# Kernel tuning notes

Hardware: AMD Instinct MI355X
Metric: run time of the kernel (lower is better)

Reference implementation:

```python
import jax, jax.numpy as jnp
import numpy as np

NUM_HEADS = 16


def trinity_mask(txt_tok, img_tok):
    """Boolean [N, N] mask, True = attend. Faithful to get_mask(..., 'trinity'):
    - image rows attend block-diagonally within 3 equal image chunks
    - text rows attend to all image tokens and causally to text tokens.
    """
    assert img_tok % 3 == 0, "Invalid text token sizes"
    sit = img_tok // 3
    N = txt_tok + img_tok
    i = jnp.arange(N)[:, None]
    j = jnp.arange(N)[None, :]
    img_img = (i < img_tok) & (j < img_tok) & ((i // sit) == (j // sit))
    txt_img = (i >= img_tok) & (j < img_tok)
    txt_txt = (i >= img_tok) & (j >= img_tok) & (i >= j)
    return img_img | txt_img | txt_txt


def setup_inputs() -> dict:
    key = jax.random.key(0)
    ks = jax.random.split(key, 12)
    B, TXT, IMG = 4, 512, 1536
    N = TXT + IMG
    DQ, DKV = 1024, 1024
    s = lambda d: 1.0 / np.sqrt(d).astype(np.float32)
    return {
        "q": jax.random.normal(ks[0], (B, N, DQ), jnp.float32),
        "kv": jax.random.normal(ks[1], (B, N, DKV), jnp.float32),
        "Wq": jax.random.normal(ks[2], (DQ, DQ), jnp.float32) * s(DQ),
        "bq": jnp.zeros((DQ,), jnp.float32),
        "Wk": jax.random.normal(ks[3], (DKV, DQ), jnp.float32) * s(DKV),
        "bk": jnp.zeros((DQ,), jnp.float32),
        "Wv": jax.random.normal(ks[4], (DKV, DQ), jnp.float32) * s(DKV),
        "bv": jnp.zeros((DQ,), jnp.float32),
        "Wo": jax.random.normal(ks[5], (DQ, DQ), jnp.float32) * s(DQ),
        "bo": jnp.zeros((DQ,), jnp.float32),
        "txt_tok_len": TXT,
        "img_tok_len": IMG,
    }


def reference(q, kv, Wq, bq, Wk, bk, Wv, bv, Wo, bo, txt_tok_len, img_tok_len):
    B, N, C = q.shape
    H = NUM_HEADS
    d = C // H
    scale = d ** -0.5
    # projections, split heads: [B, H, N, d]
    qh = (q @ Wq + bq).reshape(B, N, H, d).transpose(0, 2, 1, 3)
    kh = (kv @ Wk + bk).reshape(B, N, H, d).transpose(0, 2, 1, 3)
    vh = (kv @ Wv + bv).reshape(B, N, H, d).transpose(0, 2, 1, 3)
    scores = jnp.einsum("bhqd,bhkd->bhqk", qh, kh) * scale
    mask = trinity_mask(txt_tok_len, img_tok_len)  # [N, N] bool
    scores = jnp.where(mask[None, None], scores, -jnp.inf)
    attn = jax.nn.softmax(scores, axis=-1)
    # dropout in eval mode -> identity
    out = jnp.einsum("bhqk,bhkd->bhqd", attn, vh)
    out = out.transpose(0, 2, 1, 3).reshape(B, N, C)
    return out @ Wo + bo
```

## Files before the change

kernel.cpp:

```cpp
#include <hip/hip_runtime.h>


typedef _Float16 h16;
typedef _Float16 f16x8 __attribute__((ext_vector_type(8)));
typedef float f32x4 __attribute__((ext_vector_type(4)));

#define BATCH 4
#define NTOK  2048
#define CDIM  1024
#define NHEAD 16
#define HDIM  64
#define IMGTOK 1536
#define MROWS (BATCH * NTOK)

__device__ __forceinline__ void gload_lds16(const void* g, void* l) {
  __builtin_amdgcn_global_load_lds(
      (const __attribute__((address_space(1))) unsigned int*)g,
      (__attribute__((address_space(3))) unsigned int*)l, 16, 0, 0);
}

__global__ __launch_bounds__(256)
void cvt_f16(const float* __restrict__ s, h16* __restrict__ d) {
  size_t i = ((size_t)blockIdx.x * 256 + threadIdx.x) * 8;
  float4 a = *(const float4*)(s + i);
  float4 b = *(const float4*)(s + i + 4);
  f16x8 o;
  o[0] = (h16)a.x; o[1] = (h16)a.y; o[2] = (h16)a.z; o[3] = (h16)a.w;
  o[4] = (h16)b.x; o[5] = (h16)b.y; o[6] = (h16)b.z; o[7] = (h16)b.w;
  *(f16x8*)(d + i) = o;
}

__global__ __launch_bounds__(256)
void wtrans(const float* __restrict__ W0, const float* __restrict__ W1,
            const float* __restrict__ W2, const float* __restrict__ W3,
            h16* __restrict__ T0, h16* __restrict__ T1,
            h16* __restrict__ T2, h16* __restrict__ T3) {
  const float* W; h16* T;
  switch (blockIdx.z) {
    case 0: W = W0; T = T0; break;
    case 1: W = W1; T = T1; break;
    case 2: W = W2; T = T2; break;
    default: W = W3; T = T3; break;
  }
  __shared__ float t[32][33];
  const int n0 = blockIdx.x * 32, k0 = blockIdx.y * 32;
  const int tx = threadIdx.x, ty = threadIdx.y;
#pragma unroll
  for (int i = 0; i < 4; i++)
    t[ty + 8 * i][tx] = W[(size_t)(k0 + ty + 8 * i) * CDIM + n0 + tx];
  __syncthreads();
#pragma unroll
  for (int i = 0; i < 4; i++)
    T[(size_t)(n0 + ty + 8 * i) * CDIM + k0 + tx] = (h16)t[tx][ty + 8 * i];
}

template <int MODE>
__global__ __launch_bounds__(256)
void gemm_bt(const h16* __restrict__ X, const h16* __restrict__ WT,
             const float* __restrict__ bias, void* __restrict__ outp) {
  __shared__ __attribute__((aligned(16))) h16 smem[4 * 8192];
  const int tid = threadIdx.x;
  const int lane = tid & 63;
  const int w = tid >> 6;
  const int wr = w >> 1, wc = w & 1;
  const int l15 = lane & 15, lhi = lane >> 4;
  const int m0 = blockIdx.y * 128;
  const int n0 = blockIdx.x * 128;

  f32x4 acc[4][4] = {};

  const int sr = tid >> 2;
  const int pc = tid & 3;
  const int lc = pc ^ ((sr >> 1) & 3);
  const h16* gA0 = X + (size_t)(m0 + sr) * CDIM + lc * 8;
  const h16* gA1 = gA0 + (size_t)64 * CDIM;
  const h16* gB0 = WT + (size_t)(n0 + sr) * CDIM + lc * 8;
  const h16* gB1 = gB0 + (size_t)64 * CDIM;

#define GSTAGE(bi, kt)                                      \
  do {                                                      \
    h16* A_ = smem + (bi) * 8192;                           \
    h16* B_ = A_ + 4096;                                    \
    gload_lds16(gA0 + (kt) * 32, A_ + tid * 8);             \
    gload_lds16(gA1 + (kt) * 32, A_ + (256 + tid) * 8);     \
    gload_lds16(gB0 + (kt) * 32, B_ + tid * 8);             \
    gload_lds16(gB1 + (kt) * 32, B_ + (256 + tid) * 8);     \
  } while (0)

  const int NT = CDIM / 32;
  GSTAGE(0, 0);
  GSTAGE(1, 1);
  GSTAGE(2, 2);
  const int rswz = (l15 >> 1) & 3;

  for (int kt = 0; kt < NT; ++kt) {
    if (kt + 2 < NT)      asm volatile("s_waitcnt vmcnt(8)" ::: "memory");
    else if (kt + 1 < NT) asm volatile("s_waitcnt vmcnt(4)" ::: "memory");
    else                  asm volatile("s_waitcnt vmcnt(0)" ::: "memory");
    __builtin_amdgcn_s_barrier();
    if (kt + 3 < NT) GSTAGE((kt + 3) & 3, kt + 3);
    const h16* A_ = smem + (kt & 3) * 8192;
    const h16* B_ = A_ + 4096;
    f16x8 a[4], bb[4];
#pragma unroll
    for (int i = 0; i < 4; i++)
      a[i] = *(const f16x8*)(A_ + (wr * 64 + i * 16 + l15) * 32 + (lhi ^ rswz) * 8);
#pragma unroll
    for (int i = 0; i < 4; i++)
      bb[i] = *(const f16x8*)(B_ + (wc * 64 + i * 16 + l15) * 32 + (lhi ^ rswz) * 8);
    __builtin_amdgcn_s_setprio(1);
#pragma unroll
    for (int i = 0; i < 4; i++)
#pragma unroll
      for (int j = 0; j < 4; j++)
        acc[i][j] = __builtin_amdgcn_mfma_f32_16x16x32_f16(a[i], bb[j], acc[i][j], 0, 0, 0);
    __builtin_amdgcn_s_setprio(0);
  }
#undef GSTAGE

  if constexpr (MODE == 2) {
    __builtin_amdgcn_s_barrier();
    h16* T = smem;
#pragma unroll
    for (int j = 0; j < 4; j++) {
      const int gcL = wc * 64 + j * 16 + l15;
      const float bval = bias[n0 + gcL];
#pragma unroll
      for (int i = 0; i < 4; i++) {
#pragma unroll
        for (int r = 0; r < 4; r++) {
          const int grL = wr * 64 + i * 16 + lhi * 4 + r;
          const int ch = (grL >> 3) ^ (gcL & 15);
          T[gcL * 128 + ch * 8 + (grL & 7)] = (h16)(acc[i][j][r] + bval);
        }
      }
    }
    __builtin_amdgcn_s_barrier();
    const int bsel = m0 >> 11;
    const int nbase = m0 & (NTOK - 1);
    h16* outh = (h16*)outp;
#pragma unroll
    for (int pass = 0; pass < 8; ++pass) {
      const int rowL = pass * 16 + (tid >> 4);
      const int c = tid & 15;
      const int gc = n0 + rowL;
      const int hh = gc >> 6, dd = gc & 63;
      f16x8 v = *(const f16x8*)(T + rowL * 128 + ((c ^ (rowL & 15)) * 8));
      *(f16x8*)(outh + (((size_t)(bsel * NHEAD + hh)) * HDIM + dd) * NTOK +
                nbase + c * 8) = v;
    }
    return;
  }

#pragma unroll
  for (int j = 0; j < 4; j++) {
    const int gc = n0 + wc * 64 + j * 16 + l15;
    const float bval = bias[gc];
#pragma unroll
    for (int i = 0; i < 4; i++) {
      const int grb = m0 + wr * 64 + i * 16 + lhi * 4;
#pragma unroll
      for (int r = 0; r < 4; r++) {
        const float v = acc[i][j][r] + bval;
        const int gr = grb + r;
        if constexpr (MODE == 0) {
          ((float*)outp)[(size_t)gr * CDIM + gc] = v;
        } else {
          const int bidx = gr >> 11, n = gr & (NTOK - 1);
          const int hh = gc >> 6, dd = gc & 63;
          ((h16*)outp)[(((size_t)(bidx * NHEAD + hh)) * NTOK + n) * HDIM + dd] = (h16)v;
        }
      }
    }
  }
}

__global__ __launch_bounds__(256)
void attn_kernel(const h16* __restrict__ Qh, const h16* __restrict__ Kh,
                 const h16* __restrict__ VTh, h16* __restrict__ AX) {
  __shared__ __attribute__((aligned(16))) h16 Kb[2][64 * 64];
  __shared__ __attribute__((aligned(16))) h16 Vb[2][64 * 64];
  __shared__ __attribute__((aligned(16))) h16 Pl[4][16 * 64];

  const int tid = threadIdx.x;
  const int lane = tid & 63;
  const int w = tid >> 6;
  const int l15 = lane & 15, lhi = lane >> 4;

  const int id = blockIdx.x;
  const int pos = id >> 3;
  const int bh = (id & 7) * 8 + (pos >> 5);
  const int qblk = 31 - (pos & 31);
  const int b = bh >> 4, h = bh & 15;
  const int q0 = qblk * 64;

  const h16* qbase = Qh + (size_t)bh * NTOK * HDIM;
  const h16* kbase = Kh + (size_t)bh * NTOK * HDIM;
  const h16* vbase = VTh + (size_t)bh * HDIM * NTOK;

  const int qrow = q0 + w * 16 + l15;
  const f16x8 qf0 = *(const f16x8*)(qbase + (size_t)qrow * HDIM + lhi * 8);
  const f16x8 qf1 = *(const f16x8*)(qbase + (size_t)qrow * HDIM + 32 + lhi * 8);

  const bool is_img = (q0 < IMGTOK);
  int kstart, kend;
  if (is_img) { kstart = q0 & ~511; kend = kstart + 512; }
  else        { kstart = 0;         kend = q0 + 64; }
  const int nt = (kend - kstart) >> 6;

  float m_r[4], lp[4];
  f32x4 o[4] = {};
#pragma unroll
  for (int r = 0; r < 4; r++) { m_r[r] = -3.0e38f; lp[r] = 0.f; }

  const int srow = tid >> 3;
  const int scc = (tid & 7) ^ (srow & 7);
#define ASTAGE(bufi, k0s)                                                     \
  do {                                                                        \
    gload_lds16(kbase + (size_t)((k0s) + srow) * HDIM + scc * 8,              \
                Kb[bufi] + tid * 8);                                          \
    gload_lds16(kbase + (size_t)((k0s) + 32 + srow) * HDIM + scc * 8,         \
                Kb[bufi] + (256 + tid) * 8);                                  \
    gload_lds16(vbase + (size_t)srow * NTOK + (k0s) + scc * 8,                \
                Vb[bufi] + tid * 8);                                          \
    gload_lds16(vbase + (size_t)(32 + srow) * NTOK + (k0s) + scc * 8,         \
                Vb[bufi] + (256 + tid) * 8);                                  \
  } while (0)

  h16* pl = &Pl[w][0];
  const float sc = 0.125f * 1.44269504088896f;
  const int x0 = (lhi ^ (l15 & 7)) * 8;
  const int x1 = ((lhi + 4) ^ (l15 & 7)) * 8;

  ASTAGE(0, kstart);
  asm volatile("s_waitcnt vmcnt(0)" ::: "memory");
  __builtin_amdgcn_s_barrier();
  int cur = 0;

  for (int t = 0; t < nt; ++t) {
    const int k0 = kstart + t * 64;
    if (t + 1 < nt) ASTAGE(cur ^ 1, kstart + (t + 1) * 64);

    const h16* Kc = Kb[cur];
    f32x4 s[4];
    __builtin_amdgcn_s_setprio(1);
#pragma unroll
    for (int hk = 0; hk < 4; ++hk) {
      const h16* kr = Kc + (hk * 16 + l15) * 64;
      const f16x8 kfa = *(const f16x8*)(kr + x0);
      const f16x8 kfb = *(const f16x8*)(kr + x1);
      f32x4 acc = {};
      acc = __builtin_amdgcn_mfma_f32_16x16x32_f16(qf0, kfa, acc, 0, 0, 0);
      acc = __builtin_amdgcn_mfma_f32_16x16x32_f16(qf1, kfb, acc, 0, 0, 0);
      s[hk] = acc;
    }
    __builtin_amdgcn_s_setprio(0);

    const bool need_mask = (!is_img) && (k0 + 63 >= IMGTOK);
    float sv[4][4], lmax[4];
    bool hit = false;
#pragma unroll
    for (int r = 0; r < 4; ++r) {
#pragma unroll
      for (int hk = 0; hk < 4; ++hk) sv[r][hk] = s[hk][r] * sc;
      if (need_mask) {
        const int qg = q0 + w * 16 + lhi * 4 + r;
#pragma unroll
        for (int hk = 0; hk < 4; ++hk) {
          const int kg = k0 + hk * 16 + l15;
          if (kg >= IMGTOK && kg > qg) sv[r][hk] = -1e30f;
        }
      }
      lmax[r] = fmaxf(fmaxf(sv[r][0], sv[r][1]), fmaxf(sv[r][2], sv[r][3]));
      hit |= (lmax[r] > m_r[r] + 8.0f);
    }
    if (__any(hit)) {
#pragma unroll
      for (int r = 0; r < 4; ++r) {
        float vmax = lmax[r];
        vmax = fmaxf(vmax, __shfl_xor(vmax, 1));
        vmax = fmaxf(vmax, __shfl_xor(vmax, 2));
        vmax = fmaxf(vmax, __shfl_xor(vmax, 4));
        vmax = fmaxf(vmax, __shfl_xor(vmax, 8));
        const float mnew = fmaxf(m_r[r], vmax);
        const float corr = exp2f(m_r[r] - mnew);
        m_r[r] = mnew;
        lp[r] *= corr;
#pragma unroll
        for (int dt = 0; dt < 4; dt++) o[dt][r] *= corr;
      }
    }
#pragma unroll
    for (int r = 0; r < 4; ++r) {
      const int prow = lhi * 4 + r;
      h16* pr = pl + prow * 64;
      float rs = 0.f;
#pragma unroll
      for (int hk = 0; hk < 4; ++hk) {
        const float p = exp2f(sv[r][hk] - m_r[r]);
        rs += p;
        const int c = hk * 16 + l15;
        pr[((c >> 3) ^ (prow & 7)) * 8 + (c & 7)] = (h16)p;
      }
      lp[r] += rs;
    }
    asm volatile("s_waitcnt lgkmcnt(0)" ::: "memory");
    __builtin_amdgcn_sched_barrier(0);

    const h16* Vc = Vb[cur];
    const f16x8 pf0 = *(const f16x8*)(pl + l15 * 64 + x0);
    const f16x8 pf1 = *(const f16x8*)(pl + l15 * 64 + x1);
    __builtin_amdgcn_s_setprio(1);
#pragma unroll
    for (int dt = 0; dt < 4; dt++) {
      const h16* vr = Vc + (dt * 16 + l15) * 64;
      const f16x8 vfa = *(const f16x8*)(vr + x0);
      const f16x8 vfb = *(const f16x8*)(vr + x1);
      o[dt] = __builtin_amdgcn_mfma_f32_16x16x32_f16(pf0, vfa, o[dt], 0, 0, 0);
      o[dt] = __builtin_amdgcn_mfma_f32_16x16x32_f16(pf1, vfb, o[dt], 0, 0, 0);
    }
    __builtin_amdgcn_s_setprio(0);

    asm volatile("s_waitcnt vmcnt(0)" ::: "memory");
    __builtin_amdgcn_s_barrier();
    cur ^= 1;
  }
#undef ASTAGE

  const int qg0 = q0 + w * 16 + lhi * 4;
#pragma unroll
  for (int r = 0; r < 4; r++) {
    float l = lp[r];
    l += __shfl_xor(l, 1);
    l += __shfl_xor(l, 2);
    l += __shfl_xor(l, 4);
    l += __shfl_xor(l, 8);
    const float inv = 1.0f / l;
    const size_t row = (size_t)(b * NTOK + qg0 + r);
#pragma unroll
    for (int dt = 0; dt < 4; dt++) {
      const int col = h * 64 + dt * 16 + l15;
      AX[row * CDIM + col] = (h16)(o[dt][r] * inv);
    }
  }
}

extern "C" void kernel_launch(void* const* d_in, const int* in_sizes, int n_in,
                              void* d_out, int out_size, void* d_ws, size_t ws_size,
                              hipStream_t stream) {
  (void)in_sizes; (void)n_in; (void)out_size; (void)ws_size;
  const float* q  = (const float*)d_in[0];
  const float* kv = (const float*)d_in[1];
  const float* Wq = (const float*)d_in[2];
  const float* bq = (const float*)d_in[3];
  const float* Wk = (const float*)d_in[4];
  const float* bk = (const float*)d_in[5];
  const float* Wv = (const float*)d_in[6];
  const float* bv = (const float*)d_in[7];
  const float* Wo = (const float*)d_in[8];
  const float* bo = (const float*)d_in[9];
  float* out = (float*)d_out;

  char* ws = (char*)d_ws;
  const size_t SZ_MK = (size_t)MROWS * CDIM * sizeof(h16);
  const size_t SZ_W  = (size_t)CDIM * CDIM * sizeof(h16);
  h16* qb  = (h16*)(ws);
  h16* kvb = (h16*)(ws + SZ_MK);
  h16* wqt = (h16*)(ws + 2 * SZ_MK);
  h16* wkt = (h16*)(ws + 2 * SZ_MK + SZ_W);
  h16* wvt = (h16*)(ws + 2 * SZ_MK + 2 * SZ_W);
  h16* wot = (h16*)(ws + 2 * SZ_MK + 3 * SZ_W);
  h16* Qh  = (h16*)(ws + 2 * SZ_MK + 4 * SZ_W);
  h16* Kh  = (h16*)(ws + 3 * SZ_MK + 4 * SZ_W);
  h16* VTh = (h16*)(ws + 4 * SZ_MK + 4 * SZ_W);
  h16* ax  = (h16*)(ws);

  cvt_f16<<<4096, 256, 0, stream>>>(q, qb);
  cvt_f16<<<4096, 256, 0, stream>>>(kv, kvb);
  wtrans<<<dim3(32, 32, 4), dim3(32, 8), 0, stream>>>(Wq, Wk, Wv, Wo,
                                                      wqt, wkt, wvt, wot);
  gemm_bt<1><<<dim3(8, 64), 256, 0, stream>>>(qb, wqt, bq, (void*)Qh);
  gemm_bt<1><<<dim3(8, 64), 256, 0, stream>>>(kvb, wkt, bk, (void*)Kh);
  gemm_bt<2><<<dim3(8, 64), 256, 0, stream>>>(kvb, wvt, bv, (void*)VTh);
  attn_kernel<<<2048, 256, 0, stream>>>(Qh, Kh, VTh, ax);
  gemm_bt<0><<<dim3(8, 64), 256, 0, stream>>>(ax, wot, bo, (void*)out);
}
```

Measured before the change: 339.6 us.

## Fold softmax scale into Q projection, transpose QK^T MFMA, shrink GEMM pipeline

The Q projection now multiplies by scale*log2e in its epilogue (new MODE 3), so the attention kernel no longer scales its scores. The QK^T MFMA operands are swapped, giving each lane one query row; row max and row sum then need two cross-lane shuffles instead of four, and P is written to LDS as packed fp16 pairs. Separately, the GEMM drops from four to three LDS stages with a launch bound of three blocks per SM, aiming for higher occupancy at the cost of a shallower prefetch. Risks include the modulo-3 buffer rotation logic and extra shuffles needed to broadcast the correction factors.

```diff
diff --git a/kernel.cpp b/kernel.cpp
--- a/kernel.cpp
+++ b/kernel.cpp
@@ -3,6 +3,7 @@
 
 typedef _Float16 h16;
 typedef _Float16 f16x8 __attribute__((ext_vector_type(8)));
+typedef __fp16 fp16v2 __attribute__((ext_vector_type(2)));
 typedef float f32x4 __attribute__((ext_vector_type(4)));
 
 #define BATCH 4
@@ -12,6 +13,7 @@
 #define HDIM  64
 #define IMGTOK 1536
 #define MROWS (BATCH * NTOK)
+#define QSCALE 0.18033688011112042f
 
 __device__ __forceinline__ void gload_lds16(const void* g, void* l) {
   __builtin_amdgcn_global_load_lds(
@@ -55,10 +57,10 @@
 }
 
 template <int MODE>
-__global__ __launch_bounds__(256)
+__global__ __launch_bounds__(256, 3)
 void gemm_bt(const h16* __restrict__ X, const h16* __restrict__ WT,
              const float* __restrict__ bias, void* __restrict__ outp) {
-  __shared__ __attribute__((aligned(16))) h16 smem[4 * 8192];
+  __shared__ __attribute__((aligned(16))) h16 smem[3 * 8192];
   const int tid = threadIdx.x;
   const int lane = tid & 63;
   const int w = tid >> 6;
@@ -90,17 +92,17 @@
   const int NT = CDIM / 32;
   GSTAGE(0, 0);
   GSTAGE(1, 1);
-  GSTAGE(2, 2);
   const int rswz = (l15 >> 1) & 3;
 
+  int rb = 0, sb = 2;
   for (int kt = 0; kt < NT; ++kt) {
-    if (kt + 2 < NT)      asm volatile("s_waitcnt vmcnt(8)" ::: "memory");
-    else if (kt + 1 < NT) asm volatile("s_waitcnt vmcnt(4)" ::: "memory");
-    else                  asm volatile("s_waitcnt vmcnt(0)" ::: "memory");
+    if (kt + 1 < NT) asm volatile("s_waitcnt vmcnt(4)" ::: "memory");
+    else             asm volatile("s_waitcnt vmcnt(0)" ::: "memory");
     __builtin_amdgcn_s_barrier();
-    if (kt + 3 < NT) GSTAGE((kt + 3) & 3, kt + 3);
-    const h16* A_ = smem + (kt & 3) * 8192;
+    if (kt + 2 < NT) { GSTAGE(sb, kt + 2); sb = (sb == 2) ? 0 : sb + 1; }
+    const h16* A_ = smem + rb * 8192;
     const h16* B_ = A_ + 4096;
+    rb = (rb == 2) ? 0 : rb + 1;
     f16x8 a[4], bb[4];
 #pragma unroll
     for (int i = 0; i < 4; i++)
@@ -161,7 +163,8 @@
       const int grb = m0 + wr * 64 + i * 16 + lhi * 4;
 #pragma unroll
       for (int r = 0; r < 4; r++) {
-        const float v = acc[i][j][r] + bval;
+        float v = acc[i][j][r] + bval;
+        if constexpr (MODE == 3) v *= QSCALE;
         const int gr = grb + r;
         if constexpr (MODE == 0) {
           ((float*)outp)[(size_t)gr * CDIM + gc] = v;
@@ -186,6 +189,7 @@
   const int lane = tid & 63;
   const int w = tid >> 6;
   const int l15 = lane & 15, lhi = lane >> 4;
+  const int lhi4 = lhi * 4;
 
   const int id = blockIdx.x;
   const int pos = id >> 3;
@@ -201,6 +205,7 @@
   const int qrow = q0 + w * 16 + l15;
   const f16x8 qf0 = *(const f16x8*)(qbase + (size_t)qrow * HDIM + lhi * 8);
   const f16x8 qf1 = *(const f16x8*)(qbase + (size_t)qrow * HDIM + 32 + lhi * 8);
+  const int qg = qrow;
 
   const bool is_img = (q0 < IMGTOK);
   int kstart, kend;
@@ -208,10 +213,8 @@
   else        { kstart = 0;         kend = q0 + 64; }
   const int nt = (kend - kstart) >> 6;
 
-  float m_r[4], lp[4];
+  float m = -3.0e38f, lp = 0.f;
   f32x4 o[4] = {};
-#pragma unroll
-  for (int r = 0; r < 4; r++) { m_r[r] = -3.0e38f; lp[r] = 0.f; }
 
   const int srow = tid >> 3;
   const int scc = (tid & 7) ^ (srow & 7);
@@ -228,9 +231,12 @@
   } while (0)
 
   h16* pl = &Pl[w][0];
-  const float sc = 0.125f * 1.44269504088896f;
   const int x0 = (lhi ^ (l15 & 7)) * 8;
   const int x1 = ((lhi + 4) ^ (l15 & 7)) * 8;
+  const int pswz = l15 & 7;
+  const int phalf = (lhi & 1) * 4;
+  const int plhi2 = lhi >> 1;
+  h16* prb = pl + l15 * 64;
 
   ASTAGE(0, kstart);
   asm volatile("s_waitcnt vmcnt(0)" ::: "memory");
@@ -250,59 +256,57 @@
       const f16x8 kfa = *(const f16x8*)(kr + x0);
       const f16x8 kfb = *(const f16x8*)(kr + x1);
       f32x4 acc = {};
-      acc = __builtin_amdgcn_mfma_f32_16x16x32_f16(qf0, kfa, acc, 0, 0, 0);
-      acc = __builtin_amdgcn_mfma_f32_16x16x32_f16(qf1, kfb, acc, 0, 0, 0);
+      acc = __builtin_amdgcn_mfma_f32_16x16x32_f16(kfa, qf0, acc, 0, 0, 0);
+      acc = __builtin_amdgcn_mfma_f32_16x16x32_f16(kfb, qf1, acc, 0, 0, 0);
       s[hk] = acc;
     }
     __builtin_amdgcn_s_setprio(0);
 
     const bool need_mask = (!is_img) && (k0 + 63 >= IMGTOK);
-    float sv[4][4], lmax[4];
-    bool hit = false;
-#pragma unroll
-    for (int r = 0; r < 4; ++r) {
-#pragma unroll
-      for (int hk = 0; hk < 4; ++hk) sv[r][hk] = s[hk][r] * sc;
-      if (need_mask) {
-        const int qg = q0 + w * 16 + lhi * 4 + r;
-#pragma unroll
-        for (int hk = 0; hk < 4; ++hk) {
-          const int kg = k0 + hk * 16 + l15;
-          if (kg >= IMGTOK && kg > qg) sv[r][hk] = -1e30f;
+    float sv[4][4];
+    float lmax = -3.0e38f;
+#pragma unroll
+    for (int hk = 0; hk < 4; ++hk) {
+#pragma unroll
+      for (int r = 0; r < 4; ++r) {
+        float v = s[hk][r];
+        if (need_mask) {
+          const int kg = k0 + hk * 16 + lhi4 + r;
+          if (kg >= IMGTOK && kg > qg) v = -1e30f;
         }
+        sv[hk][r] = v;
+        lmax = fmaxf(lmax, v);
       }
-      lmax[r] = fmaxf(fmaxf(sv[r][0], sv[r][1]), fmaxf(sv[r][2], sv[r][3]));
-      hit |= (lmax[r] > m_r[r] + 8.0f);
-    }
-    if (__any(hit)) {
-#pragma unroll
-      for (int r = 0; r < 4; ++r) {
-        float vmax = lmax[r];
-        vmax = fmaxf(vmax, __shfl_xor(vmax, 1));
-        vmax = fmaxf(vmax, __shfl_xor(vmax, 2));
-        vmax = fmaxf(vmax, __shfl_xor(vmax, 4));
-        vmax = fmaxf(vmax, __shfl_xor(vmax, 8));
-        const float mnew = fmaxf(m_r[r], vmax);
-        const float corr = exp2f(m_r[r] - mnew);
-        m_r[r] = mnew;
-        lp[r] *= corr;
-#pragma unroll
-        for (int dt = 0; dt < 4; dt++) o[dt][r] *= corr;
+    }
+    if (__any(lmax > m + 8.0f)) {
+      float vmax = fmaxf(lmax, __shfl_xor(lmax, 16));
+      vmax = fmaxf(vmax, __shfl_xor(vmax, 32));
+      const float mnew = fmaxf(m, vmax);
+      const float corr = exp2f(m - mnew);
+      m = mnew;
+      lp *= corr;
+      const float c0 = __shfl(corr, lhi4 + 0);
+      const float c1 = __shfl(corr, lhi4 + 1);
+      const float c2 = __shfl(corr, lhi4 + 2);
+      const float c3 = __shfl(corr, lhi4 + 3);
+#pragma unroll
+      for (int dt = 0; dt < 4; dt++) {
+        o[dt][0] *= c0; o[dt][1] *= c1; o[dt][2] *= c2; o[dt][3] *= c3;
       }
     }
 #pragma unroll
-    for (int r = 0; r < 4; ++r) {
-      const int prow = lhi * 4 + r;
-      h16* pr = pl + prow * 64;
-      float rs = 0.f;
-#pragma unroll
-      for (int hk = 0; hk < 4; ++hk) {
-        const float p = exp2f(sv[r][hk] - m_r[r]);
-        rs += p;
-        const int c = hk * 16 + l15;
-        pr[((c >> 3) ^ (prow & 7)) * 8 + (c & 7)] = (h16)p;
-      }
-      lp[r] += rs;
+    for (int hk = 0; hk < 4; ++hk) {
+      const float e0 = exp2f(sv[hk][0] - m);
+      const float e1 = exp2f(sv[hk][1] - m);
+      const float e2 = exp2f(sv[hk][2] - m);
+      const float e3 = exp2f(sv[hk][3] - m);
+      lp += (e0 + e1) + (e2 + e3);
+      const fp16v2 lo2 = __builtin_amdgcn_cvt_pkrtz(e0, e1);
+      const fp16v2 hi2 = __builtin_amdgcn_cvt_pkrtz(e2, e3);
+      uint2 qw;
+      qw.x = __builtin_bit_cast(unsigned int, lo2);
+      qw.y = __builtin_bit_cast(unsigned int, hi2);
+      *(uint2*)(prb + ((hk * 2 + plhi2) ^ pswz) * 8 + phalf) = qw;
     }
     asm volatile("s_waitcnt lgkmcnt(0)" ::: "memory");
     __builtin_amdgcn_sched_barrier(0);
@@ -327,15 +331,14 @@
   }
 #undef ASTAGE
 
-  const int qg0 = q0 + w * 16 + lhi * 4;
+  float l = lp;
+  l += __shfl_xor(l, 16);
+  l += __shfl_xor(l, 32);
+  const int qg0 = q0 + w * 16 + lhi4;
 #pragma unroll
   for (int r = 0; r < 4; r++) {
-    float l = lp[r];
-    l += __shfl_xor(l, 1);
-    l += __shfl_xor(l, 2);
-    l += __shfl_xor(l, 4);
-    l += __shfl_xor(l, 8);
-    const float inv = 1.0f / l;
+    const float lr = __shfl(l, lhi4 + r);
+    const float inv = 1.0f / lr;
     const size_t row = (size_t)(b * NTOK + qg0 + r);
 #pragma unroll
     for (int dt = 0; dt < 4; dt++) {
@@ -379,7 +382,7 @@
   cvt_f16<<<4096, 256, 0, stream>>>(kv, kvb);
   wtrans<<<dim3(32, 32, 4), dim3(32, 8), 0, stream>>>(Wq, Wk, Wv, Wo,
                                                       wqt, wkt, wvt, wot);
-  gemm_bt<1><<<dim3(8, 64), 256, 0, stream>>>(qb, wqt, bq, (void*)Qh);
+  gemm_bt<3><<<dim3(8, 64), 256, 0, stream>>>(qb, wqt, bq, (void*)Qh);
   gemm_bt<1><<<dim3(8, 64), 256, 0, stream>>>(kvb, wkt, bk, (void*)Kh);
   gemm_bt<2><<<dim3(8, 64), 256, 0, stream>>>(kvb, wvt, bv, (void*)VTh);
   attn_kernel<<<2048, 256, 0, stream>>>(Qh, Kh, VTh, ax);
```

Measured after the change: 329.1 us. 3.1% less time.
